# Kernel tuning notes

Measured on AMD Instinct MI355X. Metric: run time of the kernel, lower is better.

Reference implementation:

```python
import jax, jax.numpy as jnp
import numpy as np

B, S, D, H, DFF = 8, 1024, 1024, 16, 4096
DK = D // H
EPS = 1e-6
NEG = -1e9


def _layer_norm(x, gamma, beta):
    # Faithful to hand-rolled LN: torch std is unbiased (ddof=1), eps added to sigma.
    mu = jnp.mean(x, axis=-1, keepdims=True)
    sigma = jnp.std(x, axis=-1, keepdims=True, ddof=1)
    return gamma * (x - mu) / (EPS + sigma) + beta


def setup_inputs() -> dict:
    key = jax.random.key(0)
    ks = jax.random.split(key, 12)
    s = 0.02
    inp = {
        "x": jax.random.normal(ks[0], (B, S, D), dtype=jnp.float32),
        "src_mask": jnp.ones((B, 1, 1, S), dtype=jnp.int32),
        "Wq": jax.random.normal(ks[1], (D, D), dtype=jnp.float32) * s,
        "bq": jnp.zeros((D,), dtype=jnp.float32),
        "Wk": jax.random.normal(ks[2], (D, D), dtype=jnp.float32) * s,
        "bk": jnp.zeros((D,), dtype=jnp.float32),
        "Wv": jax.random.normal(ks[3], (D, D), dtype=jnp.float32) * s,
        "bv": jnp.zeros((D,), dtype=jnp.float32),
        "Wo": jax.random.normal(ks[4], (D, D), dtype=jnp.float32) * s,
        "bo": jnp.zeros((D,), dtype=jnp.float32),
        "W1": jax.random.normal(ks[5], (DFF, D), dtype=jnp.float32) * s,
        "b1": jnp.zeros((DFF,), dtype=jnp.float32),
        "W2": jax.random.normal(ks[6], (D, DFF), dtype=jnp.float32) * s,
        "b2": jnp.zeros((D,), dtype=jnp.float32),
        "g1": jnp.ones((1,), dtype=jnp.float32),
        "be1": jnp.zeros((1,), dtype=jnp.float32),
        "g2": jnp.ones((1,), dtype=jnp.float32),
        "be2": jnp.zeros((1,), dtype=jnp.float32),
    }
    return inp


def _encoder_block(x, src_mask, Wq, bq, Wk, bk, Wv, bv, Wo, bo,
                   W1, b1, W2, b2, g1, be1, g2, be2):
    # Multi-head self-attention (dropout = identity in eval)
    def split(h):  # [B,S,D] -> [B,H,S,DK]
        return h.reshape(B, S, H, DK).transpose(0, 2, 1, 3)

    q = split(x @ Wq.T + bq)
    k = split(x @ Wk.T + bk)
    v = split(x @ Wv.T + bv)

    scores = jnp.einsum("bhqd,bhkd->bhqk", q, k) / jnp.sqrt(jnp.float32(DK))
    scores = jnp.where(src_mask == 0, NEG, scores)
    probs = jax.nn.softmax(scores, axis=-1)
    attn = jnp.einsum("bhqk,bhkd->bhqd", probs, v)
    attn = attn.transpose(0, 2, 1, 3).reshape(B, S, D)
    attn = attn @ Wo.T + bo

    x1 = _layer_norm(x + attn, g1, be1)

    ff = jax.nn.relu(x1 @ W1.T + b1) @ W2.T + b2
    x2 = _layer_norm(x1 + ff, g2, be2)
    return x2


def reference(x, src_mask, Wq, bq, Wk, bk, Wv, bv, Wo, bo,
              W1, b1, W2, b2, g1, be1, g2, be2):
    return _encoder_block(x, src_mask, Wq, bq, Wk, bk, Wv, bv, Wo, bo,
                          W1, b1, W2, b2, g1, be1, g2, be2)
```

## Files before the change

### kernel.cpp

```cpp
#include <hip/hip_runtime.h>
#include <stdint.h>

#define BB 8
#define SS 1024
#define DD 1024
#define HH 16
#define DFF 4096
#define MT (BB*SS)

typedef __attribute__((ext_vector_type(8))) short bf16x8;
typedef __attribute__((ext_vector_type(4))) short s16x4;
typedef __attribute__((ext_vector_type(4))) float f32x4;
typedef __attribute__((ext_vector_type(16))) float f32x16;
typedef unsigned int u32x2 __attribute__((ext_vector_type(2)));

#define LOG2E 1.44269504088896340736f

__device__ __forceinline__ short f2bf(float f) {
  union { float f; uint32_t u; } v; v.f = f;
  uint32_t r = v.u + 0x7FFFu + ((v.u >> 16) & 1u);
  return (short)(r >> 16);
}

__device__ __forceinline__ void gload_lds16(const void* g, void* l) {
  __builtin_amdgcn_global_load_lds(
      (__attribute__((address_space(1))) uint32_t*)(uintptr_t)g,
      (__attribute__((address_space(3))) uint32_t*)(uint32_t)(uintptr_t)l,
      16, 0, 0);
}

__device__ __forceinline__ uint32_t cvtpk(float lo, float hi) {
  uint32_t r;
  asm("v_cvt_pk_bf16_f32 %0, %1, %2" : "=v"(r) : "v"(lo), "v"(hi));
  return r;
}

__device__ __forceinline__ void swap2(uint32_t a, uint32_t b, uint32_t& x, uint32_t& y) {
#if __has_builtin(__builtin_amdgcn_permlane32_swap)
  u32x2 r = __builtin_amdgcn_permlane32_swap(a, b, false, false);
  x = r.x; y = r.y;
#else
  uint32_t asw = (uint32_t)__shfl_xor((int)a, 32, 64);
  uint32_t bsw = (uint32_t)__shfl_xor((int)b, 32, 64);
  bool h = (threadIdx.x & 32) != 0;
  x = h ? bsw : a;
  y = h ? b : asw;
#endif
}

__global__ __launch_bounds__(256) void cvt_bf16(const float* __restrict__ in,
                                                short* __restrict__ out, int n8) {
  int i = blockIdx.x * 256 + threadIdx.x;
  if (i >= n8) return;
  f32x4 a = *(const f32x4*)(in + (size_t)i * 8);
  f32x4 b = *(const f32x4*)(in + (size_t)i * 8 + 4);
  bf16x8 o;
  o[0]=f2bf(a[0]); o[1]=f2bf(a[1]); o[2]=f2bf(a[2]); o[3]=f2bf(a[3]);
  o[4]=f2bf(b[0]); o[5]=f2bf(b[1]); o[6]=f2bf(b[2]); o[7]=f2bf(b[3]);
  *(bf16x8*)(out + (size_t)i * 8) = o;
}

template<int BM, int RELU, int RES, int OUTF, int OUTB, int QKV>
__global__ __launch_bounds__(512, 2) void gemm_ring(
    const short* __restrict__ A, const short* __restrict__ W,
    const float* __restrict__ bq, const float* __restrict__ bk,
    const float* __restrict__ bv, const float* __restrict__ res,
    float* __restrict__ outF, short* __restrict__ outB,
    int M, int N, int K, float qscale)
{
  constexpr int AISS   = BM / 128;
  constexpr int SLOT_A = BM * 32 * 2;
  constexpr int SLOT   = SLOT_A + 256 * 32 * 2;
  constexpr int MI     = BM / 32;
  __shared__ __align__(16) char lds[3 * SLOT];

  const int tid = threadIdx.x, lane = tid & 63, wid = tid >> 6;
  const int wm = wid >> 2, wn = wid & 3;
  const int lrow = lane & 15, lk = lane >> 4;

  const int nwg = gridDim.x;
  const int cpx = nwg >> 3;
  const int id  = blockIdx.x;
  const int wg  = (id & 7) * cpx + (id >> 3);
  const int gx  = N >> 8;
  const int bx  = wg % gx, by = wg / gx;
  const int row0 = by * BM, col0 = bx * 256;

  const int lineo = lane >> 3;
  const int rin   = lineo * 2 + ((lane >> 2) & 1);
  const int ksrc  = (lane & 3) ^ (lineo & 3);

  const short* Asrc[AISS];
#pragma unroll
  for (int j = 0; j < AISS; ++j)
    Asrc[j] = A + (size_t)(row0 + (wid * AISS + j) * 16 + rin) * K + ksrc * 8;
  const short* Bsrc[2];
#pragma unroll
  for (int j = 0; j < 2; ++j)
    Bsrc[j] = W + (size_t)(col0 + (wid * 2 + j) * 16 + rin) * K + ksrc * 8;

  const f32x4 z4 = {0.f, 0.f, 0.f, 0.f};
  f32x4 acc[MI][4];
#pragma unroll
  for (int i = 0; i < MI; ++i)
#pragma unroll
    for (int j = 0; j < 4; ++j) acc[i][j] = z4;

  const int NT = K >> 5;

  auto stage = [&](int ts, int s) {
    char* base = lds + s * SLOT;
    int ko = ts * 32;
#pragma unroll
    for (int j = 0; j < AISS; ++j)
      gload_lds16(Asrc[j] + ko, base + (wid * AISS + j) * 1024);
#pragma unroll
    for (int j = 0; j < 2; ++j)
      gload_lds16(Bsrc[j] + ko, base + SLOT_A + (wid * 2 + j) * 1024);
  };

  stage(0, 0);
  stage(1, 1);

  const int laneterm = (lrow >> 1) * 128 + (lrow & 1) * 64 + ((lk ^ ((lrow >> 1) & 3)) * 16);

  int sr = 0;
  for (int t = 0; t < NT; ++t) {
    const int sw = (sr == 0) ? 2 : sr - 1;
    const int ts = (t + 2 < NT) ? t + 2 : NT - 1;
    stage(ts, sw);
    if (AISS == 2) asm volatile("s_waitcnt vmcnt(8)" ::: "memory");
    else           asm volatile("s_waitcnt vmcnt(6)" ::: "memory");
    __builtin_amdgcn_s_barrier();
    __builtin_amdgcn_sched_barrier(0);

    const char* As = lds + sr * SLOT;
    const char* Bs = As + SLOT_A;
    bf16x8 af[MI], bfr[4];
#pragma unroll
    for (int mi = 0; mi < MI; ++mi)
      af[mi] = *(const bf16x8*)(As + wm * (BM * 32) + mi * 1024 + laneterm);
#pragma unroll
    for (int ni = 0; ni < 4; ++ni)
      bfr[ni] = *(const bf16x8*)(Bs + wn * 4096 + ni * 1024 + laneterm);

    __builtin_amdgcn_s_setprio(1);
#pragma unroll
    for (int mi = 0; mi < MI; ++mi)
#pragma unroll
      for (int ni = 0; ni < 4; ++ni)
        acc[mi][ni] = __builtin_amdgcn_mfma_f32_16x16x32_bf16(af[mi], bfr[ni], acc[mi][ni], 0, 0, 0);
    __builtin_amdgcn_s_setprio(0);

    __builtin_amdgcn_s_barrier();
    sr = (sr == 2) ? 0 : sr + 1;
  }

  const int sel    = QKV ? (col0 >> 10) : 0;
  const float* bias = QKV ? (sel == 0 ? bq : (sel == 1 ? bk : bv)) : bq;
  const int strideN = QKV ? 1024 : N;
  short* outBp = OUTB ? (outB + (QKV ? (size_t)sel * MT * DD : 0)) : outB;
  const float scl = (QKV && sel == 0) ? qscale : 1.f;

#pragma unroll
  for (int mi = 0; mi < MI; ++mi) {
#pragma unroll
    for (int ni = 0; ni < 4; ++ni) {
      int col  = col0 + wn * 64 + ni * 16 + lrow;
      int coll = QKV ? (col & 1023) : col;
      float bvv = bias[coll];
#pragma unroll
      for (int r = 0; r < 4; ++r) {
        int row = row0 + wm * (BM / 2) + mi * 16 + lk * 4 + r;
        float v = acc[mi][ni][r] + bvv;
        if (QKV) v *= scl;
        if (RELU) v = fmaxf(v, 0.f);
        size_t idx = (size_t)row * strideN + coll;
        if (RES)  v += res[idx];
        if (OUTF) outF[idx] = v;
        if (OUTB) outBp[idx] = f2bf(v);
      }
    }
  }
}

__global__ __launch_bounds__(256) void transpose_v(const short* __restrict__ Vb,
                                                   short* __restrict__ Vt) {
  const int s = blockIdx.x * 256 + threadIdx.x;
  const int u = blockIdx.y;
  const int bh = blockIdx.z, b = bh >> 4, h = bh & 15;
  bf16x8 v = *(const bf16x8*)(Vb + ((size_t)(b * SS + s)) * DD + h * 64 + u * 8);
  size_t ob = ((size_t)bh * 64 + u * 8) * SS + s;
#pragma unroll
  for (int j = 0; j < 8; ++j) Vt[ob + (size_t)j * SS] = v[j];
}

__global__ __launch_bounds__(256) void attn_flash3(
    const short* __restrict__ Qm, const short* __restrict__ Km,
    const short* __restrict__ Vtg, const int* __restrict__ mask,
    short* __restrict__ Om)
{
  __shared__ short KsB[2 * 64 * 64];
  __shared__ short VsB[2 * 64 * 64];
  __shared__ float ma_all[SS];
  __shared__ float fb[4 * 32];

  const int tid = threadIdx.x, lane = tid & 63, wid = tid >> 6;
  const int l31 = lane & 31, hi = lane >> 5;
  const int bh = blockIdx.y, b = bh >> 4, h = bh & 15;
  const int q0 = blockIdx.x * 128 + wid * 32;

  {
    const int* mrow = mask + b * SS;
#pragma unroll
    for (int i = 0; i < 4; ++i) {
      int idx = i * 256 + tid;
      ma_all[idx] = (mrow[idx] == 0) ? -1.442695e9f : 0.f;
    }
  }

  bf16x8 qf[4];
  {
    const short* qrow = Qm + ((size_t)(b * SS + q0 + l31)) * DD + h * 64;
#pragma unroll
    for (int t = 0; t < 4; ++t) qf[t] = *(const bf16x8*)(qrow + t * 16 + hi * 8);
  }

  f32x16 acc0, acc1;
#pragma unroll
  for (int i = 0; i < 16; ++i) { acc0[i] = 0.f; acc1[i] = 0.f; }
  float m_r = -3e38f, l_r = 0.f;

  const int srow = tid >> 3;
  const int su = tid & 7;

  auto stageKV = [&](int kt2, int bi) {
#pragma unroll
    for (int i = 0; i < 2; ++i) {
      int r = i * 32 + srow;
      int uu = su ^ (r & 7);
      gload_lds16(Km + ((size_t)(b * SS + kt2 + r)) * DD + h * 64 + uu * 8,
                  KsB + bi * 4096 + (i * 256 + wid * 64) * 8);
      gload_lds16(Vtg + ((size_t)(bh * 64 + r)) * SS + kt2 + uu * 8,
                  VsB + bi * 4096 + (i * 256 + wid * 64) * 8);
    }
  };

  __syncthreads();
  stageKV(0, 0);

  for (int t = 0; t < 16; ++t) {
    if (t < 15) {
      stageKV((t + 1) << 6, (t + 1) & 1);
      asm volatile("s_waitcnt vmcnt(4)" ::: "memory");
    } else {
      asm volatile("s_waitcnt vmcnt(0)" ::: "memory");
    }
    __builtin_amdgcn_s_barrier();
    __builtin_amdgcn_sched_barrier(0);

    const short* Ks = KsB + (t & 1) * 4096;
    const short* Vs = VsB + (t & 1) * 4096;

    f32x16 s0, s1;
#pragma unroll
    for (int i = 0; i < 16; ++i) { s0[i] = 0.f; s1[i] = 0.f; }
#pragma unroll
    for (int t4 = 0; t4 < 4; ++t4) {
      int u = (t4 * 2 + hi) ^ (l31 & 7);
      bf16x8 k0 = *(const bf16x8*)(Ks + l31 * 64 + u * 8);
      bf16x8 k1 = *(const bf16x8*)(Ks + (32 + l31) * 64 + u * 8);
      s0 = __builtin_amdgcn_mfma_f32_32x32x16_bf16(k0, qf[t4], s0, 0, 0, 0);
      s1 = __builtin_amdgcn_mfma_f32_32x32x16_bf16(k1, qf[t4], s1, 0, 0, 0);
    }

    const float* map = ma_all + (t << 6);
    float p0[16], p1[16];
    float mx = -3e38f;
#pragma unroll
    for (int g = 0; g < 4; ++g) {
      f32x4 a0 = *(const f32x4*)(map + g * 8 + hi * 4);
      f32x4 a1 = *(const f32x4*)(map + 32 + g * 8 + hi * 4);
#pragma unroll
      for (int j = 0; j < 4; ++j) {
        float v0 = s0[g * 4 + j] + a0[j];
        float v1 = s1[g * 4 + j] + a1[j];
        p0[g * 4 + j] = v0; p1[g * 4 + j] = v1;
        mx = fmaxf(mx, fmaxf(v0, v1));
      }
    }
    mx = fmaxf(mx, __shfl_xor(mx, 32, 64));

    if (!__all(mx <= m_r + 8.f)) {
      float mn  = fmaxf(m_r, mx);
      float fac = exp2f(m_r - mn);
      m_r = mn;
      l_r *= fac;
      fb[wid * 32 + l31] = fac;
#pragma unroll
      for (int g = 0; g < 4; ++g) {
        f32x4 fv = *(const f32x4*)(fb + wid * 32 + g * 8 + hi * 4);
#pragma unroll
        for (int j = 0; j < 4; ++j) { acc0[g * 4 + j] *= fv[j]; acc1[g * 4 + j] *= fv[j]; }
      }
    }

    float rs = 0.f;
#pragma unroll
    for (int r = 0; r < 16; ++r) {
      p0[r] = exp2f(p0[r] - m_r);
      p1[r] = exp2f(p1[r] - m_r);
      rs += p0[r] + p1[r];
    }
    rs += __shfl_xor(rs, 32, 64);
    l_r += rs;

    uint32_t w0[8], w1[8];
#pragma unroll
    for (int m = 0; m < 8; ++m) {
      w0[m] = cvtpk(p0[2 * m], p0[2 * m + 1]);
      w1[m] = cvtpk(p1[2 * m], p1[2 * m + 1]);
    }
    uint32_t pa[4][4];
    swap2(w0[0], w0[2], pa[0][0], pa[0][2]);
    swap2(w0[1], w0[3], pa[0][1], pa[0][3]);
    swap2(w0[4], w0[6], pa[1][0], pa[1][2]);
    swap2(w0[5], w0[7], pa[1][1], pa[1][3]);
    swap2(w1[0], w1[2], pa[2][0], pa[2][2]);
    swap2(w1[1], w1[3], pa[2][1], pa[2][3]);
    swap2(w1[4], w1[6], pa[3][0], pa[3][2]);
    swap2(w1[5], w1[7], pa[3][1], pa[3][3]);

#pragma unroll
    for (int kc = 0; kc < 4; ++kc) {
      union { uint32_t w[4]; bf16x8 v; } pu;
      pu.w[0] = pa[kc][0]; pu.w[1] = pa[kc][1]; pu.w[2] = pa[kc][2]; pu.w[3] = pa[kc][3];
      int u = (kc * 2 + hi) ^ (l31 & 7);
      bf16x8 v0 = *(const bf16x8*)(Vs + l31 * 64 + u * 8);
      bf16x8 v1 = *(const bf16x8*)(Vs + (32 + l31) * 64 + u * 8);
      acc0 = __builtin_amdgcn_mfma_f32_32x32x16_bf16(pu.v, v0, acc0, 0, 0, 0);
      acc1 = __builtin_amdgcn_mfma_f32_32x32x16_bf16(pu.v, v1, acc1, 0, 0, 0);
    }

    __builtin_amdgcn_s_barrier();
  }

  fb[wid * 32 + l31] = 1.f / l_r;
#pragma unroll
  for (int g = 0; g < 4; ++g) {
    f32x4 rv = *(const f32x4*)(fb + wid * 32 + g * 8 + hi * 4);
#pragma unroll
    for (int j = 0; j < 4; ++j) {
      int q = q0 + g * 8 + hi * 4 + j;
      size_t base = ((size_t)(b * SS + q)) * DD + h * 64 + l31;
      Om[base]      = f2bf(acc0[g * 4 + j] * rv[j]);
      Om[base + 32] = f2bf(acc1[g * 4 + j] * rv[j]);
    }
  }
}

template<int WRITE_BF16>
__global__ __launch_bounds__(256) void layernorm_k(
    float* __restrict__ x, short* __restrict__ xb,
    const float* __restrict__ g, const float* __restrict__ be)
{
  const int row = blockIdx.x, tid = threadIdx.x;
  float* xr = x + (size_t)row * DD;
  f32x4 a = *(const f32x4*)(xr + tid * 4);
  float s  = a[0] + a[1] + a[2] + a[3];
  float ss = a[0]*a[0] + a[1]*a[1] + a[2]*a[2] + a[3]*a[3];
#pragma unroll
  for (int o = 1; o < 64; o <<= 1) { s += __shfl_xor(s, o, 64); ss += __shfl_xor(ss, o, 64); }
  __shared__ float red[8];
  const int wid = tid >> 6, lane = tid & 63;
  if (lane == 0) { red[wid] = s; red[4 + wid] = ss; }
  __syncthreads();
  s  = red[0] + red[1] + red[2] + red[3];
  ss = red[4] + red[5] + red[6] + red[7];
  float mu  = s * (1.f / DD);
  float var = fmaxf((ss - (float)DD * mu * mu) * (1.f / (DD - 1)), 0.f);
  float inv = g[0] / (1e-6f + sqrtf(var));
  float bb  = be[0];
#pragma unroll
  for (int j = 0; j < 4; ++j) a[j] = (a[j] - mu) * inv + bb;
  *(f32x4*)(xr + tid * 4) = a;
  if (WRITE_BF16) {
    s16x4 o;
#pragma unroll
    for (int j = 0; j < 4; ++j) o[j] = f2bf(a[j]);
    *(s16x4*)(xb + (size_t)row * DD + tid * 4) = o;
  }
}

extern "C" void kernel_launch(void* const* d_in, const int* in_sizes, int n_in,
                              void* d_out, int out_size, void* d_ws, size_t ws_size,
                              hipStream_t stream) {
  const float* x    = (const float*)d_in[0];
  const int*   mask = (const int*)d_in[1];
  const float* Wq = (const float*)d_in[2];  const float* bq = (const float*)d_in[3];
  const float* Wk = (const float*)d_in[4];  const float* bk = (const float*)d_in[5];
  const float* Wv = (const float*)d_in[6];  const float* bv = (const float*)d_in[7];
  const float* Wo = (const float*)d_in[8];  const float* bo = (const float*)d_in[9];
  const float* W1 = (const float*)d_in[10]; const float* b1 = (const float*)d_in[11];
  const float* W2 = (const float*)d_in[12]; const float* b2 = (const float*)d_in[13];
  const float* g1 = (const float*)d_in[14]; const float* be1 = (const float*)d_in[15];
  const float* g2 = (const float*)d_in[16]; const float* be2 = (const float*)d_in[17];
  float* out = (float*)d_out;

  char* ws = (char*)d_ws;
  size_t off = 0;
  auto alloc = [&](size_t bytes) -> char* {
    char* p = ws + off; off += (bytes + 255) & ~(size_t)255; return p;
  };
  short* xb  = (short*)alloc((size_t)MT * DD * 2);
  short* wqb = (short*)alloc((size_t)DD * DD * 2);
  short* wkb = (short*)alloc((size_t)DD * DD * 2);
  short* wvb = (short*)alloc((size_t)DD * DD * 2);
  short* wob = (short*)alloc((size_t)DD * DD * 2);
  short* w1b = (short*)alloc((size_t)DFF * DD * 2);
  short* w2b = (short*)alloc((size_t)DD * DFF * 2);
  short* Qb  = (short*)alloc((size_t)MT * DD * 2);
  short* Kb  = (short*)alloc((size_t)MT * DD * 2);
  short* Vb  = (short*)alloc((size_t)MT * DD * 2);
  short* Ab  = (short*)alloc((size_t)MT * DD * 2);
  float* x1  = (float*)alloc((size_t)MT * DD * 4);
  short* F1  = Qb;
  short* x1b = xb;
  short* Vt  = (short*)x1;
  (void)wkb; (void)wvb; (void)Kb; (void)Vb;

  const float qscale = 0.125f * LOG2E;

  cvt_bf16<<<(MT * DD / 8 + 255) / 256, 256, 0, stream>>>(x, xb, MT * DD / 8);
  cvt_bf16<<<(DD * DD / 8 + 255) / 256, 256, 0, stream>>>(Wq, wqb, DD * DD / 8);
  cvt_bf16<<<(DD * DD / 8 + 255) / 256, 256, 0, stream>>>(Wk, wkb, DD * DD / 8);
  cvt_bf16<<<(DD * DD / 8 + 255) / 256, 256, 0, stream>>>(Wv, wvb, DD * DD / 8);
  cvt_bf16<<<(DD * DD / 8 + 255) / 256, 256, 0, stream>>>(Wo, wob, DD * DD / 8);
  cvt_bf16<<<(DFF * DD / 8 + 255) / 256, 256, 0, stream>>>(W1, w1b, DFF * DD / 8);
  cvt_bf16<<<(DD * DFF / 8 + 255) / 256, 256, 0, stream>>>(W2, w2b, DD * DFF / 8);

  gemm_ring<128,0,0,0,1,1><<<dim3((3072/256)*(MT/128)), 512, 0, stream>>>(
      xb, wqb, bq, bk, bv, nullptr, nullptr, Qb, MT, 3072, DD, qscale);

  transpose_v<<<dim3(SS/256, 8, BB*HH), 256, 0, stream>>>(Vb, Vt);
  attn_flash3<<<dim3(SS/128, BB*HH), 256, 0, stream>>>(Qb, Kb, Vt, mask, Ab);

  gemm_ring<128,0,1,1,0,0><<<dim3((DD/256)*(MT/128)), 512, 0, stream>>>(
      Ab, wob, bo, bo, bo, x, x1, nullptr, MT, DD, DD, 1.f);
  layernorm_k<1><<<MT, 256, 0, stream>>>(x1, x1b, g1, be1);

  gemm_ring<128,1,0,0,1,0><<<dim3((DFF/256)*(MT/128)), 512, 0, stream>>>(
      x1b, w1b, b1, b1, b1, nullptr, nullptr, F1, MT, DFF, DD, 1.f);
  gemm_ring<128,0,1,1,0,0><<<dim3((DD/256)*(MT/128)), 512, 0, stream>>>(
      F1, w2b, b2, b2, b2, x1, out, nullptr, MT, DD, DFF, 1.f);
  layernorm_k<0><<<MT, 256, 0, stream>>>(out, nullptr, g2, be2);
}
```

Baseline: 386.0 us.

## Add 256x256-tile GEMM with 4-stage LDS ring and split-K FFN2 with fused LN

Adds a new gemm_2x kernel that uses 256x256 output tiles per 512-thread block and a 4-slot LDS pipeline (three stages prefetched, vmcnt waits). It replaces the 128-row ring GEMM for the fused QKV projection and FFN1 to raise operand reuse per loaded byte. The FFN2 GEMM becomes a 2-way split-K that accumulates into a zeroed fp32 buffer with atomicAdd. A new ln2_combine kernel then folds in bias, residual and the final layernorm. The split-K path adds a memset and atomic traffic, and the larger tiles halve the number of workgroups in exchange for better reuse.

```diff
diff --git a/kernel.cpp b/kernel.cpp
--- a/kernel.cpp
+++ b/kernel.cpp
@@ -58,6 +58,120 @@
   o[0]=f2bf(a[0]); o[1]=f2bf(a[1]); o[2]=f2bf(a[2]); o[3]=f2bf(a[3]);
   o[4]=f2bf(b[0]); o[5]=f2bf(b[1]); o[6]=f2bf(b[2]); o[7]=f2bf(b[3]);
   *(bf16x8*)(out + (size_t)i * 8) = o;
+}
+
+template<int RELU, int SPLITK, int QKV>
+__global__ __launch_bounds__(512, 2) void gemm_2x(
+    const short* __restrict__ A, const short* __restrict__ W,
+    const float* __restrict__ bq, const float* __restrict__ bk,
+    const float* __restrict__ bv,
+    float* __restrict__ outF, short* __restrict__ outB,
+    int M, int N, int lda, int K2, float qscale)
+{
+  __shared__ short lds[4 * 16384];
+  const int tid = threadIdx.x, lane = tid & 63, wid = tid >> 6;
+  const int wm = wid >> 2, wn = wid & 3;
+  const int lrow = lane & 15, lk = lane >> 4;
+
+  const int nwg = gridDim.x;
+  const int cpx = nwg >> 3;
+  const int id  = blockIdx.x;
+  const int wg  = (id & 7) * cpx + (id >> 3);
+  const int gx  = N >> 8;
+  const int bx  = wg % gx, by = wg / gx;
+  const int row0 = by * 256, col0 = bx * 256;
+  const int koff = SPLITK ? blockIdx.z * K2 : 0;
+
+  const int rin = lane >> 2, ku = lane & 3;
+  const short* Asrc0 = A + (size_t)(row0 + (wid * 2 + 0) * 16 + rin) * lda + koff + ku * 8;
+  const short* Asrc1 = Asrc0 + (size_t)16 * lda;
+  const short* Bsrc0 = W + (size_t)(col0 + (wid * 2 + 0) * 16 + rin) * lda + koff + ku * 8;
+  const short* Bsrc1 = Bsrc0 + (size_t)16 * lda;
+
+  const f32x4 z4 = {0.f, 0.f, 0.f, 0.f};
+  f32x4 acc[8][4];
+#pragma unroll
+  for (int i = 0; i < 8; ++i)
+#pragma unroll
+    for (int j = 0; j < 4; ++j) acc[i][j] = z4;
+
+  const int NH = K2 >> 5;
+
+  auto stage = [&](int h, int s) {
+    short* base = lds + s * 16384;
+    const int ko = h * 32;
+    gload_lds16(Asrc0 + ko, base + (wid * 2 + 0) * 512);
+    gload_lds16(Asrc1 + ko, base + (wid * 2 + 1) * 512);
+    gload_lds16(Bsrc0 + ko, base + 8192 + (wid * 2 + 0) * 512);
+    gload_lds16(Bsrc1 + ko, base + 8192 + (wid * 2 + 1) * 512);
+  };
+
+  stage(0, 0); stage(1, 1); stage(2, 2);
+
+  for (int h = 0; h < NH; ++h) {
+    const int hs = (h + 3 < NH) ? h + 3 : NH - 1;
+    stage(hs, (h + 3) & 3);
+    asm volatile("s_waitcnt vmcnt(12)" ::: "memory");
+    __builtin_amdgcn_s_barrier();
+    __builtin_amdgcn_sched_barrier(0);
+
+    const short* sb = lds + (h & 3) * 16384;
+    bf16x8 bf[4], af[8];
+#pragma unroll
+    for (int ni = 0; ni < 4; ++ni)
+      bf[ni] = *(const bf16x8*)(sb + 8192 + (wn * 64 + ni * 16 + lrow) * 32 + lk * 8);
+#pragma unroll
+    for (int mi = 0; mi < 4; ++mi)
+      af[mi] = *(const bf16x8*)(sb + (wm * 128 + mi * 16 + lrow) * 32 + lk * 8);
+
+    __builtin_amdgcn_s_setprio(1);
+#pragma unroll
+    for (int mi = 0; mi < 4; ++mi)
+#pragma unroll
+      for (int ni = 0; ni < 4; ++ni)
+        acc[mi][ni] = __builtin_amdgcn_mfma_f32_16x16x32_bf16(af[mi], bf[ni], acc[mi][ni], 0, 0, 0);
+    __builtin_amdgcn_s_setprio(0);
+
+#pragma unroll
+    for (int mi = 4; mi < 8; ++mi)
+      af[mi] = *(const bf16x8*)(sb + (wm * 128 + mi * 16 + lrow) * 32 + lk * 8);
+
+    __builtin_amdgcn_s_setprio(1);
+#pragma unroll
+    for (int mi = 4; mi < 8; ++mi)
+#pragma unroll
+      for (int ni = 0; ni < 4; ++ni)
+        acc[mi][ni] = __builtin_amdgcn_mfma_f32_16x16x32_bf16(af[mi], bf[ni], acc[mi][ni], 0, 0, 0);
+    __builtin_amdgcn_s_setprio(0);
+
+    __builtin_amdgcn_s_barrier();
+  }
+
+  const int sel    = QKV ? (col0 >> 10) : 0;
+  const float* bias = QKV ? (sel == 0 ? bq : (sel == 1 ? bk : bv)) : bq;
+  const int strideN = QKV ? 1024 : N;
+  short* outBp = outB + (QKV ? (size_t)sel * MT * DD : 0);
+  const float scl = (QKV && sel == 0) ? qscale : 1.f;
+
+#pragma unroll
+  for (int mi = 0; mi < 8; ++mi) {
+#pragma unroll
+    for (int ni = 0; ni < 4; ++ni) {
+      int col  = col0 + wn * 64 + ni * 16 + lrow;
+      int coll = QKV ? (col & 1023) : col;
+      float bvv = SPLITK ? 0.f : bias[coll];
+#pragma unroll
+      for (int r = 0; r < 4; ++r) {
+        int row = row0 + wm * 128 + mi * 16 + lk * 4 + r;
+        float v = acc[mi][ni][r] + bvv;
+        if (QKV) v *= scl;
+        if (RELU) v = fmaxf(v, 0.f);
+        size_t idx = (size_t)row * strideN + coll;
+        if (SPLITK) atomicAdd(&outF[idx], v);
+        else        outBp[idx] = f2bf(v);
+      }
+    }
+  }
 }
 
 template<int BM, int RELU, int RES, int OUTF, int OUTB, int QKV>
@@ -156,29 +270,24 @@
     sr = (sr == 2) ? 0 : sr + 1;
   }
 
-  const int sel    = QKV ? (col0 >> 10) : 0;
-  const float* bias = QKV ? (sel == 0 ? bq : (sel == 1 ? bk : bv)) : bq;
-  const int strideN = QKV ? 1024 : N;
-  short* outBp = OUTB ? (outB + (QKV ? (size_t)sel * MT * DD : 0)) : outB;
-  const float scl = (QKV && sel == 0) ? qscale : 1.f;
+  const float* bias = bq;
+  const int strideN = N;
 
 #pragma unroll
   for (int mi = 0; mi < MI; ++mi) {
 #pragma unroll
     for (int ni = 0; ni < 4; ++ni) {
       int col  = col0 + wn * 64 + ni * 16 + lrow;
-      int coll = QKV ? (col & 1023) : col;
-      float bvv = bias[coll];
+      float bvv = bias[col];
 #pragma unroll
       for (int r = 0; r < 4; ++r) {
         int row = row0 + wm * (BM / 2) + mi * 16 + lk * 4 + r;
         float v = acc[mi][ni][r] + bvv;
-        if (QKV) v *= scl;
         if (RELU) v = fmaxf(v, 0.f);
-        size_t idx = (size_t)row * strideN + coll;
+        size_t idx = (size_t)row * strideN + col;
         if (RES)  v += res[idx];
         if (OUTF) outF[idx] = v;
-        if (OUTB) outBp[idx] = f2bf(v);
+        if (OUTB) outB[idx] = f2bf(v);
       }
     }
   }
@@ -390,6 +499,36 @@
     for (int j = 0; j < 4; ++j) o[j] = f2bf(a[j]);
     *(s16x4*)(xb + (size_t)row * DD + tid * 4) = o;
   }
+}
+
+__global__ __launch_bounds__(256) void ln2_combine(
+    const float* __restrict__ P, const float* __restrict__ x1,
+    const float* __restrict__ b2, const float* __restrict__ g,
+    const float* __restrict__ be, float* __restrict__ out)
+{
+  const int row = blockIdx.x, tid = threadIdx.x;
+  f32x4 a  = *(const f32x4*)(P  + (size_t)row * DD + tid * 4);
+  f32x4 xr = *(const f32x4*)(x1 + (size_t)row * DD + tid * 4);
+  f32x4 bb4 = *(const f32x4*)(b2 + tid * 4);
+#pragma unroll
+  for (int j = 0; j < 4; ++j) a[j] = a[j] + bb4[j] + xr[j];
+  float s  = a[0] + a[1] + a[2] + a[3];
+  float ss = a[0]*a[0] + a[1]*a[1] + a[2]*a[2] + a[3]*a[3];
+#pragma unroll
+  for (int o = 1; o < 64; o <<= 1) { s += __shfl_xor(s, o, 64); ss += __shfl_xor(ss, o, 64); }
+  __shared__ float red[8];
+  const int wid = tid >> 6, lane = tid & 63;
+  if (lane == 0) { red[wid] = s; red[4 + wid] = ss; }
+  __syncthreads();
+  s  = red[0] + red[1] + red[2] + red[3];
+  ss = red[4] + red[5] + red[6] + red[7];
+  float mu  = s * (1.f / DD);
+  float var = fmaxf((ss - (float)DD * mu * mu) * (1.f / (DD - 1)), 0.f);
+  float inv = g[0] / (1e-6f + sqrtf(var));
+  float bb  = be[0];
+#pragma unroll
+  for (int j = 0; j < 4; ++j) a[j] = (a[j] - mu) * inv + bb;
+  *(f32x4*)(out + (size_t)row * DD + tid * 4) = a;
 }
 
 extern "C" void kernel_launch(void* const* d_in, const int* in_sizes, int n_in,
@@ -427,6 +566,7 @@
   short* F1  = Qb;
   short* x1b = xb;
   short* Vt  = (short*)x1;
+  float* P0  = (float*)ws;
   (void)wkb; (void)wvb; (void)Kb; (void)Vb;
 
   const float qscale = 0.125f * LOG2E;
@@ -439,8 +579,8 @@
   cvt_bf16<<<(DFF * DD / 8 + 255) / 256, 256, 0, stream>>>(W1, w1b, DFF * DD / 8);
   cvt_bf16<<<(DD * DFF / 8 + 255) / 256, 256, 0, stream>>>(W2, w2b, DD * DFF / 8);
 
-  gemm_ring<128,0,0,0,1,1><<<dim3((3072/256)*(MT/128)), 512, 0, stream>>>(
-      xb, wqb, bq, bk, bv, nullptr, nullptr, Qb, MT, 3072, DD, qscale);
+  gemm_2x<0,0,1><<<dim3((3072/256)*(MT/256), 1, 1), 512, 0, stream>>>(
+      xb, wqb, bq, bk, bv, nullptr, Qb, MT, 3072, DD, DD, qscale);
 
   transpose_v<<<dim3(SS/256, 8, BB*HH), 256, 0, stream>>>(Vb, Vt);
   attn_flash3<<<dim3(SS/128, BB*HH), 256, 0, stream>>>(Qb, Kb, Vt, mask, Ab);
@@ -449,9 +589,11 @@
       Ab, wob, bo, bo, bo, x, x1, nullptr, MT, DD, DD, 1.f);
   layernorm_k<1><<<MT, 256, 0, stream>>>(x1, x1b, g1, be1);
 
-  gemm_ring<128,1,0,0,1,0><<<dim3((DFF/256)*(MT/128)), 512, 0, stream>>>(
-      x1b, w1b, b1, b1, b1, nullptr, nullptr, F1, MT, DFF, DD, 1.f);
-  gemm_ring<128,0,1,1,0,0><<<dim3((DD/256)*(MT/128)), 512, 0, stream>>>(
-      F1, w2b, b2, b2, b2, x1, out, nullptr, MT, DD, DFF, 1.f);
-  layernorm_k<0><<<MT, 256, 0, stream>>>(out, nullptr, g2, be2);
-}
+  gemm_2x<1,0,0><<<dim3((DFF/256)*(MT/256), 1, 1), 512, 0, stream>>>(
+      x1b, w1b, b1, b1, b1, nullptr, F1, MT, DFF, DD, DD, 1.f);
+
+  hipMemsetAsync(P0, 0, (size_t)MT * DD * 4, stream);
+  gemm_2x<0,1,0><<<dim3((DD/256)*(MT/256), 1, 2), 512, 0, stream>>>(
+      F1, w2b, b2, b2, b2, P0, nullptr, MT, DD, DFF, DFF/2, 1.f);
+  ln2_combine<<<MT, 256, 0, stream>>>(P0, x1, b2, g2, be2, out);
+}
```

Measured after the change: 447.5 us. +15.9%, slower.

## Split-K the second FFN GEMM with atomic accumulation and fused LN combine

Applied to the files above, without the earlier changes.

The W2 GEMM (K=4096) is split into two K halves along grid z. Each half atomically adds fp32 partials into a zeroed workspace buffer, which doubles the block count for this GEMM. A new combine kernel then adds the bias and the x1 residual and applies the second layer norm, replacing the old epilogue and layernorm pass. The trade-off is an extra memset, atomic read-modify-write traffic to a 32MB buffer, and accumulation order that is no longer deterministic.

```diff
diff --git a/kernel.cpp b/kernel.cpp
--- a/kernel.cpp
+++ b/kernel.cpp
@@ -60,13 +60,13 @@
   *(bf16x8*)(out + (size_t)i * 8) = o;
 }
 
-template<int BM, int RELU, int RES, int OUTF, int OUTB, int QKV>
+template<int BM, int RELU, int RES, int OUTF, int OUTB, int QKV, int SPLITK>
 __global__ __launch_bounds__(512, 2) void gemm_ring(
     const short* __restrict__ A, const short* __restrict__ W,
     const float* __restrict__ bq, const float* __restrict__ bk,
     const float* __restrict__ bv, const float* __restrict__ res,
     float* __restrict__ outF, short* __restrict__ outB,
-    int M, int N, int K, float qscale)
+    int M, int N, int K, int Kc, float qscale)
 {
   constexpr int AISS   = BM / 128;
   constexpr int SLOT_A = BM * 32 * 2;
@@ -85,6 +85,7 @@
   const int gx  = N >> 8;
   const int bx  = wg % gx, by = wg / gx;
   const int row0 = by * BM, col0 = bx * 256;
+  const int koff = SPLITK ? blockIdx.z * Kc : 0;
 
   const int lineo = lane >> 3;
   const int rin   = lineo * 2 + ((lane >> 2) & 1);
@@ -93,11 +94,11 @@
   const short* Asrc[AISS];
 #pragma unroll
   for (int j = 0; j < AISS; ++j)
-    Asrc[j] = A + (size_t)(row0 + (wid * AISS + j) * 16 + rin) * K + ksrc * 8;
+    Asrc[j] = A + (size_t)(row0 + (wid * AISS + j) * 16 + rin) * K + koff + ksrc * 8;
   const short* Bsrc[2];
 #pragma unroll
   for (int j = 0; j < 2; ++j)
-    Bsrc[j] = W + (size_t)(col0 + (wid * 2 + j) * 16 + rin) * K + ksrc * 8;
+    Bsrc[j] = W + (size_t)(col0 + (wid * 2 + j) * 16 + rin) * K + koff + ksrc * 8;
 
   const f32x4 z4 = {0.f, 0.f, 0.f, 0.f};
   f32x4 acc[MI][4];
@@ -106,7 +107,7 @@
 #pragma unroll
     for (int j = 0; j < 4; ++j) acc[i][j] = z4;
 
-  const int NT = K >> 5;
+  const int NT = Kc >> 5;
 
   auto stage = [&](int ts, int s) {
     char* base = lds + s * SLOT;
@@ -168,7 +169,7 @@
     for (int ni = 0; ni < 4; ++ni) {
       int col  = col0 + wn * 64 + ni * 16 + lrow;
       int coll = QKV ? (col & 1023) : col;
-      float bvv = bias[coll];
+      float bvv = SPLITK ? 0.f : bias[coll];
 #pragma unroll
       for (int r = 0; r < 4; ++r) {
         int row = row0 + wm * (BM / 2) + mi * 16 + lk * 4 + r;
@@ -176,9 +177,13 @@
         if (QKV) v *= scl;
         if (RELU) v = fmaxf(v, 0.f);
         size_t idx = (size_t)row * strideN + coll;
-        if (RES)  v += res[idx];
-        if (OUTF) outF[idx] = v;
-        if (OUTB) outBp[idx] = f2bf(v);
+        if (SPLITK) {
+          atomicAdd(&outF[idx], v);
+        } else {
+          if (RES)  v += res[idx];
+          if (OUTF) outF[idx] = v;
+          if (OUTB) outBp[idx] = f2bf(v);
+        }
       }
     }
   }
@@ -390,6 +395,36 @@
     for (int j = 0; j < 4; ++j) o[j] = f2bf(a[j]);
     *(s16x4*)(xb + (size_t)row * DD + tid * 4) = o;
   }
+}
+
+__global__ __launch_bounds__(256) void ln2_combine(
+    const float* __restrict__ P, const float* __restrict__ x1,
+    const float* __restrict__ b2, const float* __restrict__ g,
+    const float* __restrict__ be, float* __restrict__ out)
+{
+  const int row = blockIdx.x, tid = threadIdx.x;
+  f32x4 a  = *(const f32x4*)(P  + (size_t)row * DD + tid * 4);
+  f32x4 xr = *(const f32x4*)(x1 + (size_t)row * DD + tid * 4);
+  f32x4 bb4 = *(const f32x4*)(b2 + tid * 4);
+#pragma unroll
+  for (int j = 0; j < 4; ++j) a[j] = a[j] + bb4[j] + xr[j];
+  float s  = a[0] + a[1] + a[2] + a[3];
+  float ss = a[0]*a[0] + a[1]*a[1] + a[2]*a[2] + a[3]*a[3];
+#pragma unroll
+  for (int o = 1; o < 64; o <<= 1) { s += __shfl_xor(s, o, 64); ss += __shfl_xor(ss, o, 64); }
+  __shared__ float red[8];
+  const int wid = tid >> 6, lane = tid & 63;
+  if (lane == 0) { red[wid] = s; red[4 + wid] = ss; }
+  __syncthreads();
+  s  = red[0] + red[1] + red[2] + red[3];
+  ss = red[4] + red[5] + red[6] + red[7];
+  float mu  = s * (1.f / DD);
+  float var = fmaxf((ss - (float)DD * mu * mu) * (1.f / (DD - 1)), 0.f);
+  float inv = g[0] / (1e-6f + sqrtf(var));
+  float bb  = be[0];
+#pragma unroll
+  for (int j = 0; j < 4; ++j) a[j] = (a[j] - mu) * inv + bb;
+  *(f32x4*)(out + (size_t)row * DD + tid * 4) = a;
 }
 
 extern "C" void kernel_launch(void* const* d_in, const int* in_sizes, int n_in,
@@ -427,6 +462,7 @@
   short* F1  = Qb;
   short* x1b = xb;
   short* Vt  = (short*)x1;
+  float* P0  = (float*)ws;
   (void)wkb; (void)wvb; (void)Kb; (void)Vb;
 
   const float qscale = 0.125f * LOG2E;
@@ -439,19 +475,21 @@
   cvt_bf16<<<(DFF * DD / 8 + 255) / 256, 256, 0, stream>>>(W1, w1b, DFF * DD / 8);
   cvt_bf16<<<(DD * DFF / 8 + 255) / 256, 256, 0, stream>>>(W2, w2b, DD * DFF / 8);
 
-  gemm_ring<128,0,0,0,1,1><<<dim3((3072/256)*(MT/128)), 512, 0, stream>>>(
-      xb, wqb, bq, bk, bv, nullptr, nullptr, Qb, MT, 3072, DD, qscale);
+  gemm_ring<128,0,0,0,1,1,0><<<dim3((3072/256)*(MT/128)), 512, 0, stream>>>(
+      xb, wqb, bq, bk, bv, nullptr, nullptr, Qb, MT, 3072, DD, DD, qscale);
 
   transpose_v<<<dim3(SS/256, 8, BB*HH), 256, 0, stream>>>(Vb, Vt);
   attn_flash3<<<dim3(SS/128, BB*HH), 256, 0, stream>>>(Qb, Kb, Vt, mask, Ab);
 
-  gemm_ring<128,0,1,1,0,0><<<dim3((DD/256)*(MT/128)), 512, 0, stream>>>(
-      Ab, wob, bo, bo, bo, x, x1, nullptr, MT, DD, DD, 1.f);
+  gemm_ring<128,0,1,1,0,0,0><<<dim3((DD/256)*(MT/128)), 512, 0, stream>>>(
+      Ab, wob, bo, bo, bo, x, x1, nullptr, MT, DD, DD, DD, 1.f);
   layernorm_k<1><<<MT, 256, 0, stream>>>(x1, x1b, g1, be1);
 
-  gemm_ring<128,1,0,0,1,0><<<dim3((DFF/256)*(MT/128)), 512, 0, stream>>>(
-      x1b, w1b, b1, b1, b1, nullptr, nullptr, F1, MT, DFF, DD, 1.f);
-  gemm_ring<128,0,1,1,0,0><<<dim3((DD/256)*(MT/128)), 512, 0, stream>>>(
-      F1, w2b, b2, b2, b2, x1, out, nullptr, MT, DD, DFF, 1.f);
-  layernorm_k<0><<<MT, 256, 0, stream>>>(out, nullptr, g2, be2);
-}
+  gemm_ring<128,1,0,0,1,0,0><<<dim3((DFF/256)*(MT/128)), 512, 0, stream>>>(
+      x1b, w1b, b1, b1, b1, nullptr, nullptr, F1, MT, DFF, DD, DD, 1.f);
+
+  hipMemsetAsync(P0, 0, (size_t)MT * DD * 4, stream);
+  gemm_ring<128,0,0,1,0,0,1><<<dim3((DD/256)*(MT/128), 1, 2), 512, 0, stream>>>(
+      F1, w2b, b2, b2, b2, nullptr, P0, nullptr, MT, DD, DFF, DFF/2, 1.f);
+  ln2_combine<<<MT, 256, 0, stream>>>(P0, x1, b2, g2, be2, out);
+}
```

After: 425.6 us. 10.3% more time.
